# Optimization experiments

Measured on AMD Instinct MI355X. Metric: run time of the kernel, lower is better.

Reference implementation:

```python
import jax, jax.numpy as jnp
from jax import lax
import numpy as np

M_BITS = 10      # retained mantissa bits (fp32 has 23)
BLOCK_K = 128    # accumulation block size along K


def round_mantissa(x, m_bits=M_BITS):
    """Round-to-nearest-even the fp32 mantissa to m_bits via bit manipulation.
    Exponent carry on mantissa overflow is handled naturally by integer add."""
    if m_bits >= 23:
        return x
    shift = 23 - m_bits
    b = lax.bitcast_convert_type(x, jnp.int32)
    # round-half-to-even bias: (lsb_kept) + (2^(shift-1) - 1)
    rb = ((b >> shift) & 1) + ((1 << (shift - 1)) - 1)
    b = (b + rb) & ~((1 << shift) - 1)
    return lax.bitcast_convert_type(b, jnp.float32)


def setup_inputs() -> dict:
    key = jax.random.key(0)
    k1, k2, k3 = jax.random.split(key, 3)
    M, K, N = 8192, 4096, 4096
    x = jax.random.normal(k1, (M, K), dtype=jnp.float32)
    weight = jax.random.normal(k2, (N, K), dtype=jnp.float32)  # [out, in] like torch Linear
    bias = jax.random.normal(k3, (N,), dtype=jnp.float32)
    return {"x": x, "weight": weight, "bias": bias}


def reference(x, weight, bias):
    # out = custom_accum_gemm(x, weight.T): blockwise K accumulation with
    # mantissa rounding applied to the accumulator after every block.
    M, K = x.shape
    N = weight.shape[0]
    nblk = K // BLOCK_K
    xb = x.reshape(M, nblk, BLOCK_K).transpose(1, 0, 2)        # [nblk, M, bk]
    wb = weight.T.reshape(nblk, BLOCK_K, N)                    # [nblk, bk, N]

    def step(acc, blk):
        xk, wk = blk
        acc = round_mantissa(acc + xk @ wk)
        return acc, None

    acc0 = jnp.zeros((M, N), dtype=jnp.float32)
    out, _ = lax.scan(step, acc0, (xb, wb))
    # bias add followed by mantissa rounding (as in forward)
    return round_mantissa(out + bias)
```

## Files before the change

### kernel.cpp

```cpp
#include <hip/hip_runtime.h>
#include <stdint.h>
#include <stddef.h>

typedef __attribute__((ext_vector_type(4))) float f32x4;
typedef __attribute__((ext_vector_type(16))) float f32x16;
typedef __attribute__((ext_vector_type(8))) short bf16x8;

#define BMN 256
#define BK  64
#define NTHREADS 512

__device__ __forceinline__ float round_m10(float x) {
    int b = __float_as_int(x);
    int rb = ((b >> 13) & 1) + 0x0FFF;
    b = (b + rb) & (int)0xFFFFE000;
    return __int_as_float(b);
}

__device__ __forceinline__ unsigned short f32_to_bf16(float x) {
    unsigned int u = __float_as_uint(x);
    u += 0x7FFFu + ((u >> 16) & 1u);
    return (unsigned short)(u >> 16);
}

__global__ void convert_f32_bf16_swz(const float* __restrict__ in,
                                     unsigned short* __restrict__ out,
                                     long nchunks, int cpr ) {
    long g = (long)blockIdx.x * blockDim.x + threadIdx.x;
    const long stride = (long)gridDim.x * blockDim.x;
    for (; g < nchunks; g += stride) {
        const long row = g / cpr;
        const int c = (int)(g - row * cpr);
        const float* p = in + g * 8;
        f32x4 v0 = *(const f32x4*)p;
        f32x4 v1 = *(const f32x4*)(p + 4);
        bf16x8 o;
        o[0] = (short)f32_to_bf16(v0[0]); o[1] = (short)f32_to_bf16(v0[1]);
        o[2] = (short)f32_to_bf16(v0[2]); o[3] = (short)f32_to_bf16(v0[3]);
        o[4] = (short)f32_to_bf16(v1[0]); o[5] = (short)f32_to_bf16(v1[1]);
        o[6] = (short)f32_to_bf16(v1[2]); o[7] = (short)f32_to_bf16(v1[3]);
        const int cdst = (c & ~7) | ((c & 7) ^ ((int)row & 7));
        *(bf16x8*)(out + (row * (long)cpr + cdst) * 8) = o;
    }
}

__device__ __forceinline__ void gload_lds16(const unsigned short* g, unsigned short* l) {
    __builtin_amdgcn_global_load_lds(
        (const __attribute__((address_space(1))) void*)g,
        (__attribute__((address_space(3))) void*)l, 16, 0, 0);
}

__device__ __forceinline__ void stage_half(const unsigned short* __restrict__ G,
                                           unsigned short* lds,
                                           int grow0, int gcol, int K, int tid) {
    const int wave = tid >> 6;
#pragma unroll
    for (int p = 0; p < 2; ++p) {
        const int s = tid + p * NTHREADS;
        const int row = s >> 3;
        const unsigned short* g = G + (size_t)(grow0 + row) * K + gcol + (s & 7) * 8;
        unsigned short* l = lds + (size_t)(wave * 64 + p * NTHREADS) * 8;
        gload_lds16(g, l);
    }
}

__global__ __launch_bounds__(NTHREADS, 2)
void gemm8p(const unsigned short* __restrict__ Abf, const unsigned short* __restrict__ Bbf,
            const float* __restrict__ bias, float* __restrict__ out,
            int M, int N, int K) {
    __shared__ unsigned short sA[2][2][128 * 64];
    __shared__ unsigned short sB[2][2][128 * 64];

    const int tid  = threadIdx.x;
    const int lane = tid & 63;
    const int wave = tid >> 6;
    const int wm = wave >> 2;
    const int wn = wave & 3;
    const int li = lane & 31;
    const int hi = lane >> 5;
    const int NT = K / BK;

    const int gx = gridDim.x;
    const int nwg = gx * gridDim.y;
    int lin = blockIdx.y * gx + blockIdx.x;
    if ((nwg & 7) == 0) lin = (lin & 7) * (nwg >> 3) + (lin >> 3);
    const int bm0 = (lin / gx) * BMN;
    const int bn0 = (lin % gx) * BMN;

    const int r7  = li & 7;
    const int kc0 = ((0 + hi) ^ r7) * 8;
    const int kc1 = ((2 + hi) ^ r7) * 8;
    const int kc2 = ((4 + hi) ^ r7) * 8;
    const int kc3 = ((6 + hi) ^ r7) * 8;
    const int Arow = li * 64;
    const int Brow = ((wn & 1) * 64 + li) * 64;

    const unsigned short* Ab0 = &sA[0][wm][0];
    const unsigned short* Ab1 = &sA[1][wm][0];
    const unsigned short* Bb0 = &sB[0][wn >> 1][0];
    const unsigned short* Bb1 = &sB[1][wn >> 1][0];

    f32x16 acc[8];
    {
        f32x16 z;
#pragma unroll
        for (int e = 0; e < 16; ++e) z[e] = 0.0f;
#pragma unroll
        for (int i = 0; i < 8; ++i) acc[i] = z;
    }

    bf16x8 a0[4], a1[4], b0[2], b1[2];

#define RD_A32(dst, base, kc) { const unsigned short* _pa = (base); \
    _Pragma("unroll") for (int b = 0; b < 4; ++b) \
        dst[b] = *(const bf16x8*)&_pa[b * 2048 + Arow + (kc)]; }
#define RD_B32(dst, base, kc) { const unsigned short* _pb = (base); \
    _Pragma("unroll") for (int cb = 0; cb < 2; ++cb) \
        dst[cb] = *(const bf16x8*)&_pb[cb * 2048 + Brow + (kc)]; }

#define MFMA8(aU, bU) \
    __builtin_amdgcn_s_setprio(1); \
    _Pragma("unroll") for (int b = 0; b < 4; ++b) \
    _Pragma("unroll") for (int cb = 0; cb < 2; ++cb) \
        acc[b * 2 + cb] = __builtin_amdgcn_mfma_f32_32x32x16_bf16(aU[b], bU[cb], acc[b * 2 + cb], 0, 0, 0); \
    __builtin_amdgcn_s_setprio(0);

#define PH_PLAIN(aU, bU, RDS, STG) \
    __builtin_amdgcn_sched_barrier(0); \
    STG \
    MFMA8(aU, bU) \
    RDS \
    __builtin_amdgcn_sched_barrier(0); \
    asm volatile("s_waitcnt lgkmcnt(0)"); \
    __builtin_amdgcn_s_barrier();

#define PH_PUB(aU, bU, RDS, STG, VMW) \
    __builtin_amdgcn_sched_barrier(0); \
    STG \
    VMW \
    __builtin_amdgcn_sched_barrier(0); \
    __builtin_amdgcn_s_barrier(); \
    __builtin_amdgcn_sched_barrier(0); \
    MFMA8(aU, bU) \
    RDS \
    __builtin_amdgcn_sched_barrier(0); \
    asm volatile("s_waitcnt lgkmcnt(0)"); \
    __builtin_amdgcn_s_barrier();

    stage_half(Abf, &sA[0][0][0], bm0,       0,  K, tid);
    stage_half(Abf, &sA[0][1][0], bm0 + 128, 0,  K, tid);
    stage_half(Bbf, &sB[0][0][0], bn0,       0,  K, tid);
    stage_half(Bbf, &sB[0][1][0], bn0 + 128, 0,  K, tid);
    stage_half(Abf, &sA[1][0][0], bm0,       BK, K, tid);
    stage_half(Abf, &sA[1][1][0], bm0 + 128, BK, K, tid);
    stage_half(Bbf, &sB[1][0][0], bn0,       BK, K, tid);
    stage_half(Bbf, &sB[1][1][0], bn0 + 128, BK, K, tid);
    asm volatile("s_waitcnt vmcnt(8)");
    __builtin_amdgcn_s_barrier();
    __builtin_amdgcn_sched_barrier(0);
    RD_A32(a0, Ab0, kc0)
    RD_B32(b0, Bb0, kc0)

    for (int t = 0; t < NT; t += 2) {
        int u2 = t + 2; if (u2 >= NT) u2 -= NT;
        int u3 = t + 3; if (u3 >= NT) u3 -= NT;
        const int k2 = u2 * BK, k3 = u3 * BK;

        PH_PLAIN(a0, b0,
                 RD_A32(a1, Ab0, kc1) RD_B32(b1, Bb0, kc1), )

        PH_PLAIN(a1, b1,
                 RD_A32(a0, Ab0, kc2) RD_B32(b0, Bb0, kc2), )

        PH_PLAIN(a0, b0,
                 RD_A32(a1, Ab0, kc3) RD_B32(b1, Bb0, kc3), )

        PH_PUB(a1, b1,
               RD_A32(a0, Ab1, kc0) RD_B32(b0, Bb1, kc0),
               stage_half(Abf, &sA[0][0][0], bm0, k2, K, tid);,
               asm volatile("s_waitcnt vmcnt(2)");)

        PH_PLAIN(a0, b0,
                 RD_A32(a1, Ab1, kc1) RD_B32(b1, Bb1, kc1),
                 stage_half(Abf, &sA[0][1][0], bm0 + 128, k2, K, tid);)

        PH_PLAIN(a1, b1,
                 RD_A32(a0, Ab1, kc2) RD_B32(b0, Bb1, kc2),
                 stage_half(Bbf, &sB[0][0][0], bn0, k2, K, tid);)

        PH_PLAIN(a0, b0,
                 RD_A32(a1, Ab1, kc3) RD_B32(b1, Bb1, kc3),
                 stage_half(Bbf, &sB[0][1][0], bn0 + 128, k2, K, tid);)

        PH_PUB(a1, b1,
               RD_A32(a0, Ab0, kc0) RD_B32(b0, Bb0, kc0),
               stage_half(Abf, &sA[1][0][0], bm0, k3, K, tid);
               stage_half(Abf, &sA[1][1][0], bm0 + 128, k3, K, tid);
               stage_half(Bbf, &sB[1][0][0], bn0, k3, K, tid);
               stage_half(Bbf, &sB[1][1][0], bn0 + 128, k3, K, tid);,
               asm volatile("s_waitcnt vmcnt(8)");)
    }

    asm volatile("s_waitcnt vmcnt(0) lgkmcnt(0)" ::: "memory");

#pragma unroll
    for (int b = 0; b < 4; ++b) {
        const int row0 = bm0 + wm * 128 + b * 32 + 4 * hi;
#pragma unroll
        for (int cb = 0; cb < 2; ++cb) {
            const int col = bn0 + wn * 64 + cb * 32 + li;
            const float bv = bias[col];
#pragma unroll
            for (int g = 0; g < 4; ++g)
#pragma unroll
                for (int r = 0; r < 4; ++r)
                    out[(size_t)(row0 + g * 8 + r) * N + col] =
                        round_m10(acc[b * 2 + cb][g * 4 + r] + bv);
        }
    }
#undef RD_A32
#undef RD_B32
#undef MFMA8
#undef PH_PLAIN
#undef PH_PUB
}

__global__ __launch_bounds__(256)
void gemm_fallback(const float* __restrict__ A, const float* __restrict__ B,
                   const float* __restrict__ bias, float* __restrict__ out,
                   int M, int N, int K) {
    __shared__ unsigned short lds_a[128 * 64];
    __shared__ unsigned short lds_b[128 * 64];
    const int tid = threadIdx.x, lane = tid & 63, wave = tid >> 6;
    const int wm = wave >> 1, wn = wave & 1;
    const int bm0 = blockIdx.y * 128, bn0 = blockIdx.x * 128;
    const int lrow = lane & 15, lkg = lane >> 4;
    f32x4 acc[4][4];
    const f32x4 zero = {0.f, 0.f, 0.f, 0.f};
#pragma unroll
    for (int i = 0; i < 4; ++i)
#pragma unroll
        for (int j = 0; j < 4; ++j) acc[i][j] = zero;
    for (int kb = 0; kb < K / 64; ++kb) {
        const int kt = kb * 64;
        const int r0 = tid >> 4, c0 = (tid & 15) << 2;
#pragma unroll
        for (int p = 0; p < 8; ++p) {
            const int r = p * 16 + r0;
            f32x4 va = *(const f32x4*)(A + (size_t)(bm0 + r) * K + kt + c0);
            f32x4 vb = *(const f32x4*)(B + (size_t)(bn0 + r) * K + kt + c0);
            ushort4 ua, ub;
            ua.x = f32_to_bf16(va[0]); ua.y = f32_to_bf16(va[1]);
            ua.z = f32_to_bf16(va[2]); ua.w = f32_to_bf16(va[3]);
            ub.x = f32_to_bf16(vb[0]); ub.y = f32_to_bf16(vb[1]);
            ub.z = f32_to_bf16(vb[2]); ub.w = f32_to_bf16(vb[3]);
            *(ushort4*)(&lds_a[r * 64 + c0]) = ua;
            *(ushort4*)(&lds_b[r * 64 + c0]) = ub;
        }
        __syncthreads();
#pragma unroll
        for (int kk = 0; kk < 64; kk += 32) {
            bf16x8 af[4], bfr[4];
#pragma unroll
            for (int i = 0; i < 4; ++i)
                af[i] = *(const bf16x8*)(&lds_a[(wm * 64 + i * 16 + lrow) * 64 + kk + lkg * 8]);
#pragma unroll
            for (int j = 0; j < 4; ++j)
                bfr[j] = *(const bf16x8*)(&lds_b[(wn * 64 + j * 16 + lrow) * 64 + kk + lkg * 8]);
#pragma unroll
            for (int i = 0; i < 4; ++i)
#pragma unroll
                for (int j = 0; j < 4; ++j)
                    acc[i][j] = __builtin_amdgcn_mfma_f32_16x16x32_bf16(af[i], bfr[j], acc[i][j], 0, 0, 0);
        }
        __syncthreads();
    }
#pragma unroll
    for (int i = 0; i < 4; ++i) {
        const int row0 = bm0 + wm * 64 + i * 16 + lkg * 4;
#pragma unroll
        for (int j = 0; j < 4; ++j) {
            const int col = bn0 + wn * 64 + j * 16 + lrow;
            const float bv = bias[col];
#pragma unroll
            for (int r = 0; r < 4; ++r)
                out[(size_t)(row0 + r) * N + col] = round_m10(acc[i][j][r] + bv);
        }
    }
}

extern "C" void kernel_launch(void* const* d_in, const int* in_sizes, int n_in,
                              void* d_out, int out_size, void* d_ws, size_t ws_size,
                              hipStream_t stream) {
    const float* x    = (const float*)d_in[0];
    const float* w    = (const float*)d_in[1];
    const float* bias = (const float*)d_in[2];
    float* out = (float*)d_out;

    const int N = in_sizes[2];
    const int K = in_sizes[1] / N;
    const int M = in_sizes[0] / K;

    const size_t nx = (size_t)M * K;
    const size_t nw = (size_t)N * K;
    const size_t need = (nx + nw) * sizeof(unsigned short);
    const int NT = K / BK;

    if (ws_size >= need && (M % BMN) == 0 && (N % BMN) == 0 && (K % BK) == 0 &&
        NT >= 4 && (NT % 2) == 0) {
        unsigned short* xb = (unsigned short*)d_ws;
        unsigned short* wb = xb + nx;
        const int cpr = K / 8;
        convert_f32_bf16_swz<<<2048, 256, 0, stream>>>(x, xb, (long)(nx / 8), cpr);
        convert_f32_bf16_swz<<<2048, 256, 0, stream>>>(w, wb, (long)(nw / 8), cpr);
        dim3 grid(N / BMN, M / BMN);
        gemm8p<<<grid, NTHREADS, 0, stream>>>(xb, wb, bias, out, M, N, K);
    } else {
        dim3 grid(N / 128, M / 128);
        gemm_fallback<<<grid, 256, 0, stream>>>(x, w, bias, out, M, N, K);
    }
}
```

Baseline: 334.1 us.

## Restructure GEMM main loop with one barrier per phase and deeper B prefetch

Merges the two phase macros into one macro that places a single barrier and LDS wait before each MFMA group, instead of a trailing wait and barrier after the LDS reads. B fragments are now read from LDS two phases ahead using four rotating register sets. Global-to-LDS staging is spread more evenly across the eight phases with new vmcnt thresholds. The goal is fewer barriers and stalls per phase and more overlap of LDS reads with MFMA, at the cost of more registers and a more intricate ordering of buffer reuse that could hide read-after-write hazards.

```diff
diff --git a/kernel.cpp b/kernel.cpp
--- a/kernel.cpp
+++ b/kernel.cpp
@@ -109,7 +109,7 @@
         for (int i = 0; i < 8; ++i) acc[i] = z;
     }
 
-    bf16x8 a0[4], a1[4], b0[2], b1[2];
+    bf16x8 a0[4], a1[4], bs0[2], bs1[2], bs2[2], bs3[2];
 
 #define RD_A32(dst, base, kc) { const unsigned short* _pa = (base); \
     _Pragma("unroll") for (int b = 0; b < 4; ++b) \
@@ -118,87 +118,73 @@
     _Pragma("unroll") for (int cb = 0; cb < 2; ++cb) \
         dst[cb] = *(const bf16x8*)&_pb[cb * 2048 + Brow + (kc)]; }
 
-#define MFMA8(aU, bU) \
+#define PH(aU, bU, RDS, STG, VMW) \
+    STG \
+    VMW \
+    __builtin_amdgcn_sched_barrier(0); \
+    __builtin_amdgcn_s_barrier(); \
+    asm volatile("s_waitcnt lgkmcnt(0)" ::: "memory"); \
+    __builtin_amdgcn_sched_barrier(0); \
     __builtin_amdgcn_s_setprio(1); \
     _Pragma("unroll") for (int b = 0; b < 4; ++b) \
     _Pragma("unroll") for (int cb = 0; cb < 2; ++cb) \
         acc[b * 2 + cb] = __builtin_amdgcn_mfma_f32_32x32x16_bf16(aU[b], bU[cb], acc[b * 2 + cb], 0, 0, 0); \
-    __builtin_amdgcn_s_setprio(0);
-
-#define PH_PLAIN(aU, bU, RDS, STG) \
-    __builtin_amdgcn_sched_barrier(0); \
-    STG \
-    MFMA8(aU, bU) \
-    RDS \
-    __builtin_amdgcn_sched_barrier(0); \
-    asm volatile("s_waitcnt lgkmcnt(0)"); \
-    __builtin_amdgcn_s_barrier();
-
-#define PH_PUB(aU, bU, RDS, STG, VMW) \
-    __builtin_amdgcn_sched_barrier(0); \
-    STG \
-    VMW \
-    __builtin_amdgcn_sched_barrier(0); \
-    __builtin_amdgcn_s_barrier(); \
-    __builtin_amdgcn_sched_barrier(0); \
-    MFMA8(aU, bU) \
-    RDS \
-    __builtin_amdgcn_sched_barrier(0); \
-    asm volatile("s_waitcnt lgkmcnt(0)"); \
-    __builtin_amdgcn_s_barrier();
+    __builtin_amdgcn_s_setprio(0); \
+    RDS
 
     stage_half(Abf, &sA[0][0][0], bm0,       0,  K, tid);
     stage_half(Abf, &sA[0][1][0], bm0 + 128, 0,  K, tid);
     stage_half(Bbf, &sB[0][0][0], bn0,       0,  K, tid);
     stage_half(Bbf, &sB[0][1][0], bn0 + 128, 0,  K, tid);
-    stage_half(Abf, &sA[1][0][0], bm0,       BK, K, tid);
-    stage_half(Abf, &sA[1][1][0], bm0 + 128, BK, K, tid);
     stage_half(Bbf, &sB[1][0][0], bn0,       BK, K, tid);
     stage_half(Bbf, &sB[1][1][0], bn0 + 128, BK, K, tid);
-    asm volatile("s_waitcnt vmcnt(8)");
+    asm volatile("s_waitcnt vmcnt(4)" ::: "memory");
     __builtin_amdgcn_s_barrier();
     __builtin_amdgcn_sched_barrier(0);
     RD_A32(a0, Ab0, kc0)
-    RD_B32(b0, Bb0, kc0)
+    RD_B32(bs0, Bb0, kc0)
+    RD_B32(bs1, Bb0, kc1)
 
     for (int t = 0; t < NT; t += 2) {
         int u2 = t + 2; if (u2 >= NT) u2 -= NT;
         int u3 = t + 3; if (u3 >= NT) u3 -= NT;
-        const int k2 = u2 * BK, k3 = u3 * BK;
-
-        PH_PLAIN(a0, b0,
-                 RD_A32(a1, Ab0, kc1) RD_B32(b1, Bb0, kc1), )
-
-        PH_PLAIN(a1, b1,
-                 RD_A32(a0, Ab0, kc2) RD_B32(b0, Bb0, kc2), )
-
-        PH_PLAIN(a0, b0,
-                 RD_A32(a1, Ab0, kc3) RD_B32(b1, Bb0, kc3), )
-
-        PH_PUB(a1, b1,
-               RD_A32(a0, Ab1, kc0) RD_B32(b0, Bb1, kc0),
-               stage_half(Abf, &sA[0][0][0], bm0, k2, K, tid);,
-               asm volatile("s_waitcnt vmcnt(2)");)
-
-        PH_PLAIN(a0, b0,
-                 RD_A32(a1, Ab1, kc1) RD_B32(b1, Bb1, kc1),
-                 stage_half(Abf, &sA[0][1][0], bm0 + 128, k2, K, tid);)
-
-        PH_PLAIN(a1, b1,
-                 RD_A32(a0, Ab1, kc2) RD_B32(b0, Bb1, kc2),
-                 stage_half(Bbf, &sB[0][0][0], bn0, k2, K, tid);)
-
-        PH_PLAIN(a0, b0,
-                 RD_A32(a1, Ab1, kc3) RD_B32(b1, Bb1, kc3),
-                 stage_half(Bbf, &sB[0][1][0], bn0 + 128, k2, K, tid);)
-
-        PH_PUB(a1, b1,
-               RD_A32(a0, Ab0, kc0) RD_B32(b0, Bb0, kc0),
-               stage_half(Abf, &sA[1][0][0], bm0, k3, K, tid);
-               stage_half(Abf, &sA[1][1][0], bm0 + 128, k3, K, tid);
-               stage_half(Bbf, &sB[1][0][0], bn0, k3, K, tid);
-               stage_half(Bbf, &sB[1][1][0], bn0 + 128, k3, K, tid);,
-               asm volatile("s_waitcnt vmcnt(8)");)
+        const int k1 = (t + 1) * BK, k2 = u2 * BK, k3 = u3 * BK;
+
+        PH(a0, bs0,
+           RD_A32(a1, Ab0, kc1) RD_B32(bs2, Bb0, kc2),
+           stage_half(Abf, &sA[1][0][0], bm0, k1, K, tid);, )
+
+        PH(a1, bs1,
+           RD_A32(a0, Ab0, kc2) RD_B32(bs3, Bb0, kc3),
+           stage_half(Abf, &sA[1][1][0], bm0 + 128, k1, K, tid);, )
+
+        PH(a0, bs2,
+           RD_A32(a1, Ab0, kc3) RD_B32(bs0, Bb1, kc0),
+           , asm volatile("s_waitcnt vmcnt(4)" ::: "memory");)
+
+        PH(a1, bs3,
+           RD_A32(a0, Ab1, kc0) RD_B32(bs1, Bb1, kc1),
+           stage_half(Bbf, &sB[0][0][0], bn0, k2, K, tid);,
+           asm volatile("s_waitcnt vmcnt(2)" ::: "memory");)
+
+        PH(a0, bs0,
+           RD_A32(a1, Ab1, kc1) RD_B32(bs2, Bb1, kc2),
+           stage_half(Bbf, &sB[0][1][0], bn0 + 128, k2, K, tid);, )
+
+        PH(a1, bs1,
+           RD_A32(a0, Ab1, kc2) RD_B32(bs3, Bb1, kc3),
+           stage_half(Abf, &sA[0][0][0], bm0, k2, K, tid);, )
+
+        PH(a0, bs2,
+           RD_A32(a1, Ab1, kc3) RD_B32(bs0, Bb0, kc0),
+           stage_half(Abf, &sA[0][1][0], bm0 + 128, k2, K, tid);,
+           asm volatile("s_waitcnt vmcnt(4)" ::: "memory");)
+
+        PH(a1, bs3,
+           RD_A32(a0, Ab0, kc0) RD_B32(bs1, Bb0, kc1),
+           stage_half(Bbf, &sB[1][0][0], bn0, k3, K, tid);
+           stage_half(Bbf, &sB[1][1][0], bn0 + 128, k3, K, tid);,
+           asm volatile("s_waitcnt vmcnt(4)" ::: "memory");)
     }
 
     asm volatile("s_waitcnt vmcnt(0) lgkmcnt(0)" ::: "memory");
@@ -220,9 +206,7 @@
     }
 #undef RD_A32
 #undef RD_B32
-#undef MFMA8
-#undef PH_PLAIN
-#undef PH_PUB
+#undef PH
 }
 
 __global__ __launch_bounds__(256)
```

After: 330.0 us. Within noise of the previous version (-1.2%).
